# Kernel tuning notes

Measured on AMD Instinct MI355X. Metric: run time of the kernel, lower is better.

## Reference

```python
import jax, jax.numpy as jnp
import numpy as np

DIM = 384
HEADS = 8


def conv1x1(x, w):
    # x: [b,c,h,w], w: [o,c] (1x1 conv, no bias)
    return jnp.einsum('bchw,oc->bohw', x, w)


def dwconv3x3(x, w):
    # depthwise 3x3, padding=1. x: [b,c,h,w], w: [c,1,3,3]
    return jax.lax.conv_general_dilated(
        x, w, window_strides=(1, 1), padding='SAME',
        feature_group_count=x.shape[1],
        dimension_numbers=('NCHW', 'OIHW', 'NCHW'))


def l2norm(x, eps=1e-12):
    # F.normalize(dim=-1): x / max(||x||_2, eps)
    n = jnp.sqrt(jnp.sum(x * x, axis=-1, keepdims=True))
    return x / jnp.maximum(n, eps)


def topm_softmax(attn, m):
    # keep top-m per row (by value threshold == scatter of topk indices), -inf elsewhere
    thr = jax.lax.top_k(attn, m)[0][..., -1:]
    return jax.nn.softmax(jnp.where(attn >= thr, attn, -jnp.inf), axis=-1)


def setup_inputs() -> dict:
    key = jax.random.key(0)
    ks = jax.random.split(key, 9)
    d = DIM
    return {
        'x_q': jax.random.normal(ks[0], (8, d, 128, 128), jnp.float32),
        'x_kv': jax.random.normal(ks[1], (8, d, 128, 128), jnp.float32),
        'q_w': jax.random.normal(ks[2], (d, d), jnp.float32) * 0.02,
        'q_dw': jax.random.normal(ks[3], (d, 1, 3, 3), jnp.float32) * 0.02,
        'kv_w': jax.random.normal(ks[4], (2 * d, d), jnp.float32) * 0.02,
        'kv_dw': jax.random.normal(ks[5], (2 * d, 1, 3, 3), jnp.float32) * 0.02,
        'proj_w': jax.random.normal(ks[6], (d, d), jnp.float32) * 0.02,
        'temperature': jnp.ones((HEADS, 1, 1), jnp.float32),
        'a_mix': jnp.full((4,), 0.2, jnp.float32),  # attn1..attn4
    }


def reference(x_q, x_kv, q_w, q_dw, kv_w, kv_dw, proj_w, temperature, a_mix):
    b, c, h, w = x_q.shape
    C = c // HEADS  # channels per head
    n = h * w

    q = dwconv3x3(conv1x1(x_q, q_w), q_dw)
    kv = dwconv3x3(conv1x1(x_kv, kv_w), kv_dw)
    k, v = jnp.split(kv, 2, axis=1)

    q = l2norm(q.reshape(b, HEADS, C, n))
    k = l2norm(k.reshape(b, HEADS, C, n))
    v = v.reshape(b, HEADS, C, n)

    attn = jnp.einsum('bhcn,bhdn->bhcd', q, k) * temperature  # [b,H,C,C]

    topks = (C // 2, (2 * C) // 3, (3 * C) // 4, (4 * C) // 5)
    out = jnp.zeros_like(v)
    for i, m in enumerate(topks):
        a = topm_softmax(attn, m)
        out = out + a_mix[i] * jnp.einsum('bhcd,bhdn->bhcn', a, v)

    out = out.reshape(b, c, h, w)
    return conv1x1(out, proj_w)
```

## Files before the change

kernel.cpp:

```cpp
#include <hip/hip_runtime.h>
#include <cstdint>
#include <cstddef>

#define DIM 384
#define HEADS 8
#define NBATCH 8
#define NPIX 16384
#define CPH 48

typedef unsigned short h16_t;
typedef __attribute__((ext_vector_type(8))) _Float16 half8;
typedef __attribute__((ext_vector_type(4))) float floatx4;

__device__ __forceinline__ h16_t f2h(float f) {
  _Float16 h = (_Float16)f;
  return __builtin_bit_cast(h16_t, h);
}
__device__ __forceinline__ float h2f(h16_t u) {
  return (float)__builtin_bit_cast(_Float16, u);
}

__device__ __forceinline__ void gload_lds16(const void* g, void* l) {
  __builtin_amdgcn_global_load_lds(
      (const __attribute__((address_space(1))) unsigned int*)g,
      (__attribute__((address_space(3))) unsigned int*)l, 16, 0, 0);
}

__global__ void convert_h16_kernel(const float* __restrict__ in, h16_t* __restrict__ out, int n) {
  int i = blockIdx.x * blockDim.x + threadIdx.x;
  if (i < n) out[i] = f2h(in[i]);
}

template <typename T>
__global__ __launch_bounds__(256) void transpose_conv_kernel(
    const T* __restrict__ in, h16_t* __restrict__ out, int C, int Nn) {
  __shared__ h16_t tile[64][68];
  int b = blockIdx.z;
  int c0 = blockIdx.y * 64;
  int n0 = blockIdx.x * 64;
  const T* src = in + (size_t)b * C * Nn;
  h16_t* dst = out + (size_t)b * Nn * C;
  int t = threadIdx.x;
  int cl = t >> 4;
  int n4 = (t & 15) << 2;
#pragma unroll
  for (int p = 0; p < 4; ++p) {
    int c = cl + p * 16;
    const T* sp = src + (size_t)(c0 + c) * Nn + n0 + n4;
    h16_t v0, v1, v2, v3;
    if (sizeof(T) == 4) {
      float4 f = *(const float4*)sp;
      v0 = f2h(f.x); v1 = f2h(f.y); v2 = f2h(f.z); v3 = f2h(f.w);
    } else {
      ushort4 u = *(const ushort4*)sp;
      v0 = u.x; v1 = u.y; v2 = u.z; v3 = u.w;
    }
    tile[n4 + 0][c] = v0;
    tile[n4 + 1][c] = v1;
    tile[n4 + 2][c] = v2;
    tile[n4 + 3][c] = v3;
  }
  __syncthreads();
  int nl = t >> 4;
  int c4 = (t & 15) << 2;
#pragma unroll
  for (int p = 0; p < 4; ++p) {
    int n = nl + p * 16;
    ushort4 w;
    w.x = tile[n][c4 + 0];
    w.y = tile[n][c4 + 1];
    w.z = tile[n][c4 + 2];
    w.w = tile[n][c4 + 3];
    *(ushort4*)(dst + (size_t)(n0 + n) * C + c0 + c4) = w;
  }
}

template <bool F32OUT, bool ABATCH>
__global__ __launch_bounds__(256) void gemm_bt_kernel(
    const h16_t* __restrict__ Aall, const h16_t* __restrict__ Ball, void* __restrict__ Cout) {
  __shared__ __align__(16) h16_t lds[16384];
  h16_t* lA = lds;
  h16_t* lB = lds + 8192;
  int b = blockIdx.z, mb = blockIdx.y, nb = blockIdx.x;
  const h16_t* A = Aall + (ABATCH ? (size_t)b * DIM * DIM : (size_t)0) + (size_t)mb * 128 * DIM;
  const h16_t* B = Ball + ((size_t)b * NPIX + (size_t)nb * 128) * DIM;
  int tid = threadIdx.x;
  int wid = tid >> 6, lane = tid & 63;
  int wi = wid >> 1, wj = wid & 1;
  int quad = lane >> 4, l15 = lane & 15;
  int srow = lane >> 3;
  int schunk = (lane & 7) ^ srow;

  floatx4 acc[4][4];
#pragma unroll
  for (int i = 0; i < 4; ++i)
#pragma unroll
    for (int j = 0; j < 4; ++j) acc[i][j] = (floatx4)0.0f;

  for (int kt = 0; kt < 6; ++kt) {
    __syncthreads();
#pragma unroll
    for (int t = 0; t < 4; ++t) {
      int r = (wid * 4 + t) * 8 + srow;
      const h16_t* ga = A + (size_t)r * DIM + kt * 64 + schunk * 8;
      const h16_t* gb = B + (size_t)r * DIM + kt * 64 + schunk * 8;
      char* la = (char*)lA + (wid * 4 + t) * 1024 + lane * 16;
      char* lb = (char*)lB + (wid * 4 + t) * 1024 + lane * 16;
      gload_lds16(ga, la);
      gload_lds16(gb, lb);
    }
    __syncthreads();
#pragma unroll
    for (int ks = 0; ks < 2; ++ks) {
      half8 af[4], bfr[4];
      int ph = (((ks << 2) | quad) ^ (l15 & 7)) << 4;
#pragma unroll
      for (int i = 0; i < 4; ++i)
        af[i] = *(const half8*)((const char*)lA + (wi * 64 + i * 16 + l15) * 128 + ph);
#pragma unroll
      for (int j = 0; j < 4; ++j)
        bfr[j] = *(const half8*)((const char*)lB + (wj * 64 + j * 16 + l15) * 128 + ph);
#pragma unroll
      for (int i = 0; i < 4; ++i)
#pragma unroll
        for (int j = 0; j < 4; ++j)
          acc[i][j] = __builtin_amdgcn_mfma_f32_16x16x32_f16(af[i], bfr[j], acc[i][j], 0, 0, 0);
    }
  }
  int orow0 = mb * 128 + wi * 64 + quad * 4;
  int ncol0 = nb * 128 + wj * 64 + l15;
#pragma unroll
  for (int i = 0; i < 4; ++i) {
#pragma unroll
    for (int j = 0; j < 4; ++j) {
#pragma unroll
      for (int r = 0; r < 4; ++r) {
        size_t idx = ((size_t)b * DIM + (orow0 + i * 16 + r)) * NPIX + (ncol0 + j * 16);
        if (F32OUT)
          ((float*)Cout)[idx] = acc[i][j][r];
        else
          ((h16_t*)Cout)[idx] = f2h(acc[i][j][r]);
      }
    }
  }
}

__device__ __forceinline__ void load_row6(const h16_t* ip, int yy, int x0, float* r) {
  if ((unsigned)yy > 127u) {
    r[0] = r[1] = r[2] = r[3] = r[4] = r[5] = 0.f;
    return;
  }
  const h16_t* row = ip + (yy << 7) + x0;
  ushort4 m = *(const ushort4*)row;
  r[0] = (x0 > 0) ? h2f(row[-1]) : 0.f;
  r[1] = h2f(m.x); r[2] = h2f(m.y); r[3] = h2f(m.z); r[4] = h2f(m.w);
  r[5] = (x0 < 124) ? h2f(row[4]) : 0.f;
}

__global__ __launch_bounds__(256) void dwconv_kernel(
    const h16_t* __restrict__ in, const float* __restrict__ wbase,
    h16_t* __restrict__ out, float* __restrict__ norm2) {
  int c = blockIdx.x, b = blockIdx.y;
  const h16_t* ip = in + ((size_t)(b * DIM + c) << 14);
  h16_t* op = out + ((size_t)(b * DIM + c) << 14);
  const float* wp = wbase + c * 9;
  float w0 = wp[0], w1 = wp[1], w2 = wp[2], w3 = wp[3], w4 = wp[4];
  float w5 = wp[5], w6 = wp[6], w7 = wp[7], w8 = wp[8];
  float ssum = 0.f;
  for (int t = threadIdx.x; t < 4096; t += 256) {
    int y = t >> 5;
    int x0 = (t & 31) << 2;
    float r0[6], r1[6], r2[6];
    load_row6(ip, y - 1, x0, r0);
    load_row6(ip, y,     x0, r1);
    load_row6(ip, y + 1, x0, r2);
    ushort4 st;
#pragma unroll
    for (int i = 0; i < 4; ++i) {
      float o = w0 * r0[i] + w1 * r0[i + 1] + w2 * r0[i + 2]
              + w3 * r1[i] + w4 * r1[i + 1] + w5 * r1[i + 2]
              + w6 * r2[i] + w7 * r2[i + 1] + w8 * r2[i + 2];
      h16_t ob = f2h(o);
      float of = h2f(ob);
      ssum += of * of;
      if (i == 0) st.x = ob; else if (i == 1) st.y = ob; else if (i == 2) st.z = ob; else st.w = ob;
    }
    *(ushort4*)(op + (y << 7) + x0) = st;
  }
  if (norm2 != nullptr) {
    __shared__ float red[256];
    int tid = threadIdx.x;
    red[tid] = ssum;
    __syncthreads();
    for (int s = 128; s > 0; s >>= 1) {
      if (tid < s) red[tid] += red[tid + s];
      __syncthreads();
    }
    if (tid == 0) norm2[b * DIM + c] = red[0];
  }
}

__global__ __launch_bounds__(64) void attn_gemm_kernel(
    const h16_t* __restrict__ q, const h16_t* __restrict__ k, float* __restrict__ attn) {
  int chunk = blockIdx.x, bh = blockIdx.y;
  int b = bh >> 3, h = bh & 7;
  const h16_t* qb = q + ((size_t)(b * DIM + h * CPH) << 14);
  const h16_t* kb = k + ((size_t)(b * DIM + h * CPH) << 14);
  int lane = threadIdx.x;
  int quad = lane >> 4, l15 = lane & 15;
  int off0 = chunk * 2048 + quad * 8;
  floatx4 acc[3][3];
#pragma unroll
  for (int i = 0; i < 3; ++i)
#pragma unroll
    for (int j = 0; j < 3; ++j) acc[i][j] = (floatx4)0.0f;
  for (int s = 0; s < 64; ++s) {
    int off = off0 + s * 32;
    half8 af[3], bfr[3];
#pragma unroll
    for (int i = 0; i < 3; ++i) {
      af[i]  = *(const half8*)(qb + ((size_t)(i * 16 + l15) << 14) + off);
      bfr[i] = *(const half8*)(kb + ((size_t)(i * 16 + l15) << 14) + off);
    }
#pragma unroll
    for (int i = 0; i < 3; ++i)
#pragma unroll
      for (int j = 0; j < 3; ++j)
        acc[i][j] = __builtin_amdgcn_mfma_f32_16x16x32_f16(af[i], bfr[j], acc[i][j], 0, 0, 0);
  }
  float* ap = attn + (size_t)bh * CPH * CPH;
#pragma unroll
  for (int i = 0; i < 3; ++i)
#pragma unroll
    for (int j = 0; j < 3; ++j)
#pragma unroll
      for (int r = 0; r < 4; ++r)
        atomicAdd(&ap[(i * 16 + quad * 4 + r) * CPH + j * 16 + l15], acc[i][j][r]);
}

__global__ __launch_bounds__(256) void combine_kernel(
    const float* __restrict__ attn, const float* __restrict__ n2q, const float* __restrict__ n2k,
    const float* __restrict__ temp, const float* __restrict__ amix,
    const float* __restrict__ projw, h16_t* __restrict__ Bmat) {
  int bh = blockIdx.x;
  int b = bh >> 3, h = bh & 7;
  __shared__ float Asc[CPH][CPH];
  __shared__ float Ex[CPH][CPH];
  __shared__ float thr[CPH][4];
  __shared__ float rmax[CPH];
  __shared__ float den[CPH][4];
  __shared__ float rsq[CPH], rsk[CPH];
  int tid = threadIdx.x;
  if (tid < CPH) {
    float nq = sqrtf(n2q[b * DIM + h * CPH + tid]);
    rsq[tid] = 1.f / fmaxf(nq, 1e-12f);
    float nk = sqrtf(n2k[b * DIM + h * CPH + tid]);
    rsk[tid] = 1.f / fmaxf(nk, 1e-12f);
  }
  __syncthreads();
  float tscale = temp[h];
  const float* ap = attn + (size_t)bh * CPH * CPH;
  for (int idx = tid; idx < CPH * CPH; idx += 256) {
    int c = idx / CPH, d = idx - c * CPH;
    Asc[c][d] = ap[idx] * rsq[c] * rsk[d] * tscale;
  }
  __syncthreads();
  const int M0 = 24, M1 = 32, M2 = 36, M3 = 38;
  for (int idx = tid; idx < CPH * CPH; idx += 256) {
    int c = idx / CPH, d = idx - c * CPH;
    float a = Asc[c][d];
    int gt = 0, ge = 0;
    float mx = -1e30f;
    for (int e = 0; e < CPH; ++e) {
      float v = Asc[c][e];
      gt += (v > a);
      ge += (v >= a);
      mx = fmaxf(mx, v);
    }
    if (d == 0) rmax[c] = mx;
    if (gt < M0 && ge >= M0) thr[c][0] = a;
    if (gt < M1 && ge >= M1) thr[c][1] = a;
    if (gt < M2 && ge >= M2) thr[c][2] = a;
    if (gt < M3 && ge >= M3) thr[c][3] = a;
  }
  __syncthreads();
  for (int idx = tid; idx < CPH * CPH; idx += 256) {
    int c = idx / CPH, d = idx - c * CPH;
    Ex[c][d] = expf(Asc[c][d] - rmax[c]);
  }
  __syncthreads();
  if (tid < CPH * 4) {
    int c = tid >> 2, mi = tid & 3;
    float t_ = thr[c][mi];
    float s = 0.f;
    for (int e = 0; e < CPH; ++e)
      if (Asc[c][e] >= t_) s += Ex[c][e];
    den[c][mi] = s;
  }
  __syncthreads();
  float a0 = amix[0], a1 = amix[1], a2 = amix[2], a3 = amix[3];
  for (int idx = tid; idx < CPH * CPH; idx += 256) {
    int c = idx / CPH, d = idx - c * CPH;
    float a = Asc[c][d];
    float s = 0.f;
    if (a >= thr[c][0]) s += a0 / den[c][0];
    if (a >= thr[c][1]) s += a1 / den[c][1];
    if (a >= thr[c][2]) s += a2 / den[c][2];
    if (a >= thr[c][3]) s += a3 / den[c][3];
    Ex[c][d] = Ex[c][d] * s;
  }
  __syncthreads();
  for (int idx = tid; idx < DIM * CPH; idx += 256) {
    int o = idx / CPH, d = idx - (idx / CPH) * CPH;
    const float* pw = projw + (size_t)o * DIM + h * CPH;
    float s = 0.f;
    for (int c2 = 0; c2 < CPH; ++c2) s += pw[c2] * Ex[c2][d];
    Bmat[((size_t)b * DIM + o) * DIM + h * CPH + d] = f2h(s);
  }
}

extern "C" void kernel_launch(void* const* d_in, const int* in_sizes, int n_in,
                              void* d_out, int out_size, void* d_ws, size_t ws_size,
                              hipStream_t stream) {
  const float* x_q    = (const float*)d_in[0];
  const float* x_kv   = (const float*)d_in[1];
  const float* q_w    = (const float*)d_in[2];
  const float* q_dw   = (const float*)d_in[3];
  const float* kv_w   = (const float*)d_in[4];
  const float* kv_dw  = (const float*)d_in[5];
  const float* proj_w = (const float*)d_in[6];
  const float* temp   = (const float*)d_in[7];
  const float* amix   = (const float*)d_in[8];

  char* ws = (char*)d_ws;
  const size_t SLOT = (size_t)NBATCH * NPIX * DIM * 2;
  h16_t* S0 = (h16_t*)(ws);
  h16_t* S1 = (h16_t*)(ws + SLOT);
  h16_t* S2 = (h16_t*)(ws + 2 * SLOT);
  h16_t* S3 = (h16_t*)(ws + 3 * SLOT);
  char* p = ws + 4 * SLOT;
  h16_t* WqB  = (h16_t*)p; p += (size_t)DIM * DIM * 2;
  h16_t* WkvB = (h16_t*)p; p += (size_t)2 * DIM * DIM * 2;
  float* n2q  = (float*)p;  p += (size_t)NBATCH * DIM * 4;
  float* n2k  = (float*)p;  p += (size_t)NBATCH * DIM * 4;
  float* attn = (float*)p;  p += (size_t)64 * CPH * CPH * 4;
  h16_t* Bmat = (h16_t*)p; p += (size_t)NBATCH * DIM * DIM * 2;

  hipMemsetAsync(attn, 0, (size_t)64 * CPH * CPH * 4, stream);

  convert_h16_kernel<<<dim3((DIM * DIM + 255) / 256), 256, 0, stream>>>(q_w, WqB, DIM * DIM);
  convert_h16_kernel<<<dim3((2 * DIM * DIM + 255) / 256), 256, 0, stream>>>(kv_w, WkvB, 2 * DIM * DIM);

  dim3 tgrid(NPIX / 64, DIM / 64, NBATCH);
  dim3 ggrid(NPIX / 128, DIM / 128, NBATCH);

  transpose_conv_kernel<float><<<tgrid, 256, 0, stream>>>(x_q, S0, DIM, NPIX);
  gemm_bt_kernel<false, false><<<ggrid, 256, 0, stream>>>(WqB, S0, S1);
  dwconv_kernel<<<dim3(DIM, NBATCH), 256, 0, stream>>>(S1, q_dw, S2, n2q);

  transpose_conv_kernel<float><<<tgrid, 256, 0, stream>>>(x_kv, S0, DIM, NPIX);
  gemm_bt_kernel<false, false><<<ggrid, 256, 0, stream>>>(WkvB, S0, S1);
  dwconv_kernel<<<dim3(DIM, NBATCH), 256, 0, stream>>>(S1, kv_dw, S3, n2k);

  attn_gemm_kernel<<<dim3(8, 64), 64, 0, stream>>>(S2, S3, attn);
  combine_kernel<<<dim3(64), 256, 0, stream>>>(attn, n2q, n2k, temp, amix, proj_w, Bmat);

  gemm_bt_kernel<false, false><<<ggrid, 256, 0, stream>>>(WkvB + (size_t)DIM * DIM, S0, S1);
  dwconv_kernel<<<dim3(DIM, NBATCH), 256, 0, stream>>>(S1, kv_dw + (size_t)DIM * 9, S2, nullptr);
  transpose_conv_kernel<unsigned short><<<tgrid, 256, 0, stream>>>(S2, S3, DIM, NPIX);

  gemm_bt_kernel<true, true><<<ggrid, 256, 0, stream>>>(Bmat, S3, d_out);
}
```

Measured before the change: 1.190 ms.

## Fuse transposes into GEMM B-operand loads and double attention-GEMM grid

```diff
diff --git a/kernel.cpp b/kernel.cpp
--- a/kernel.cpp
+++ b/kernel.cpp
@@ -31,65 +31,35 @@
   if (i < n) out[i] = f2h(in[i]);
 }
 
-template <typename T>
-__global__ __launch_bounds__(256) void transpose_conv_kernel(
-    const T* __restrict__ in, h16_t* __restrict__ out, int C, int Nn) {
-  __shared__ h16_t tile[64][68];
-  int b = blockIdx.z;
-  int c0 = blockIdx.y * 64;
-  int n0 = blockIdx.x * 64;
-  const T* src = in + (size_t)b * C * Nn;
-  h16_t* dst = out + (size_t)b * Nn * C;
-  int t = threadIdx.x;
-  int cl = t >> 4;
-  int n4 = (t & 15) << 2;
-#pragma unroll
-  for (int p = 0; p < 4; ++p) {
-    int c = cl + p * 16;
-    const T* sp = src + (size_t)(c0 + c) * Nn + n0 + n4;
-    h16_t v0, v1, v2, v3;
-    if (sizeof(T) == 4) {
-      float4 f = *(const float4*)sp;
-      v0 = f2h(f.x); v1 = f2h(f.y); v2 = f2h(f.z); v3 = f2h(f.w);
-    } else {
-      ushort4 u = *(const ushort4*)sp;
-      v0 = u.x; v1 = u.y; v2 = u.z; v3 = u.w;
-    }
-    tile[n4 + 0][c] = v0;
-    tile[n4 + 1][c] = v1;
-    tile[n4 + 2][c] = v2;
-    tile[n4 + 3][c] = v3;
-  }
-  __syncthreads();
-  int nl = t >> 4;
-  int c4 = (t & 15) << 2;
-#pragma unroll
-  for (int p = 0; p < 4; ++p) {
-    int n = nl + p * 16;
-    ushort4 w;
-    w.x = tile[n][c4 + 0];
-    w.y = tile[n][c4 + 1];
-    w.z = tile[n][c4 + 2];
-    w.w = tile[n][c4 + 3];
-    *(ushort4*)(dst + (size_t)(n0 + n) * C + c0 + c4) = w;
-  }
-}
-
-template <bool F32OUT, bool ABATCH>
-__global__ __launch_bounds__(256) void gemm_bt_kernel(
-    const h16_t* __restrict__ Aall, const h16_t* __restrict__ Ball, void* __restrict__ Cout) {
-  __shared__ __align__(16) h16_t lds[16384];
-  h16_t* lA = lds;
-  h16_t* lB = lds + 8192;
+template <bool F32OUT, bool ABATCH, typename BT>
+__global__ __launch_bounds__(256) void gemm_tn_kernel(
+    const h16_t* __restrict__ Aall, const BT* __restrict__ Ball, void* __restrict__ Cout) {
+  __shared__ __align__(16) h16_t lA[128 * 64];
+  __shared__ __align__(16) h16_t lB[128 * 72];
   int b = blockIdx.z, mb = blockIdx.y, nb = blockIdx.x;
   const h16_t* A = Aall + (ABATCH ? (size_t)b * DIM * DIM : (size_t)0) + (size_t)mb * 128 * DIM;
-  const h16_t* B = Ball + ((size_t)b * NPIX + (size_t)nb * 128) * DIM;
+  const BT* B = Ball + (size_t)b * DIM * NPIX + (size_t)nb * 128;
   int tid = threadIdx.x;
   int wid = tid >> 6, lane = tid & 63;
   int wi = wid >> 1, wj = wid & 1;
   int quad = lane >> 4, l15 = lane & 15;
   int srow = lane >> 3;
   int schunk = (lane & 7) ^ srow;
+  int koct = tid & 7;
+  int n4 = tid >> 3;
+
+  float4 f[8];
+  ushort4 u[8];
+  auto loadB = [&](int ktL) {
+    const BT* bp = B + (size_t)(ktL * 64 + koct * 8) * NPIX + (size_t)n4 * 4;
+#pragma unroll
+    for (int i = 0; i < 8; ++i) {
+      if constexpr (sizeof(BT) == 4)
+        f[i] = *(const float4*)(bp + (size_t)i * NPIX);
+      else
+        u[i] = *(const ushort4*)(bp + (size_t)i * NPIX);
+    }
+  };
 
   floatx4 acc[4][4];
 #pragma unroll
@@ -97,29 +67,48 @@
 #pragma unroll
     for (int j = 0; j < 4; ++j) acc[i][j] = (floatx4)0.0f;
 
+  loadB(0);
   for (int kt = 0; kt < 6; ++kt) {
     __syncthreads();
+    half8 w0, w1, w2, w3;
+#pragma unroll
+    for (int i = 0; i < 8; ++i) {
+      if constexpr (sizeof(BT) == 4) {
+        w0[i] = (_Float16)f[i].x; w1[i] = (_Float16)f[i].y;
+        w2[i] = (_Float16)f[i].z; w3[i] = (_Float16)f[i].w;
+      } else {
+        w0[i] = __builtin_bit_cast(_Float16, u[i].x);
+        w1[i] = __builtin_bit_cast(_Float16, u[i].y);
+        w2[i] = __builtin_bit_cast(_Float16, u[i].z);
+        w3[i] = __builtin_bit_cast(_Float16, u[i].w);
+      }
+    }
+    {
+      char* bb = (char*)lB + n4 * (4 * 144) + koct * 16;
+      *(half8*)(bb + 0)   = w0;
+      *(half8*)(bb + 144) = w1;
+      *(half8*)(bb + 288) = w2;
+      *(half8*)(bb + 432) = w3;
+    }
 #pragma unroll
     for (int t = 0; t < 4; ++t) {
       int r = (wid * 4 + t) * 8 + srow;
-      const h16_t* ga = A + (size_t)r * DIM + kt * 64 + schunk * 8;
-      const h16_t* gb = B + (size_t)r * DIM + kt * 64 + schunk * 8;
-      char* la = (char*)lA + (wid * 4 + t) * 1024 + lane * 16;
-      char* lb = (char*)lB + (wid * 4 + t) * 1024 + lane * 16;
-      gload_lds16(ga, la);
-      gload_lds16(gb, lb);
+      gload_lds16(A + (size_t)r * DIM + kt * 64 + schunk * 8,
+                  (char*)lA + (wid * 4 + t) * 1024 + lane * 16);
     }
     __syncthreads();
+    if (kt < 5) loadB(kt + 1);
 #pragma unroll
     for (int ks = 0; ks < 2; ++ks) {
       half8 af[4], bfr[4];
       int ph = (((ks << 2) | quad) ^ (l15 & 7)) << 4;
+      int pb = (((ks << 2) | quad)) << 4;
 #pragma unroll
       for (int i = 0; i < 4; ++i)
         af[i] = *(const half8*)((const char*)lA + (wi * 64 + i * 16 + l15) * 128 + ph);
 #pragma unroll
       for (int j = 0; j < 4; ++j)
-        bfr[j] = *(const half8*)((const char*)lB + (wj * 64 + j * 16 + l15) * 128 + ph);
+        bfr[j] = *(const half8*)((const char*)lB + (wj * 64 + j * 16 + l15) * 144 + pb);
 #pragma unroll
       for (int i = 0; i < 4; ++i)
 #pragma unroll
@@ -208,13 +197,13 @@
   const h16_t* kb = k + ((size_t)(b * DIM + h * CPH) << 14);
   int lane = threadIdx.x;
   int quad = lane >> 4, l15 = lane & 15;
-  int off0 = chunk * 2048 + quad * 8;
+  int off0 = chunk * 1024 + quad * 8;
   floatx4 acc[3][3];
 #pragma unroll
   for (int i = 0; i < 3; ++i)
 #pragma unroll
     for (int j = 0; j < 3; ++j) acc[i][j] = (floatx4)0.0f;
-  for (int s = 0; s < 64; ++s) {
+  for (int s = 0; s < 32; ++s) {
     int off = off0 + s * 32;
     half8 af[3], bfr[3];
 #pragma unroll
@@ -351,23 +340,19 @@
   convert_h16_kernel<<<dim3((DIM * DIM + 255) / 256), 256, 0, stream>>>(q_w, WqB, DIM * DIM);
   convert_h16_kernel<<<dim3((2 * DIM * DIM + 255) / 256), 256, 0, stream>>>(kv_w, WkvB, 2 * DIM * DIM);
 
-  dim3 tgrid(NPIX / 64, DIM / 64, NBATCH);
   dim3 ggrid(NPIX / 128, DIM / 128, NBATCH);
 
-  transpose_conv_kernel<float><<<tgrid, 256, 0, stream>>>(x_q, S0, DIM, NPIX);
-  gemm_bt_kernel<false, false><<<ggrid, 256, 0, stream>>>(WqB, S0, S1);
-  dwconv_kernel<<<dim3(DIM, NBATCH), 256, 0, stream>>>(S1, q_dw, S2, n2q);
-
-  transpose_conv_kernel<float><<<tgrid, 256, 0, stream>>>(x_kv, S0, DIM, NPIX);
-  gemm_bt_kernel<false, false><<<ggrid, 256, 0, stream>>>(WkvB, S0, S1);
-  dwconv_kernel<<<dim3(DIM, NBATCH), 256, 0, stream>>>(S1, kv_dw, S3, n2k);
-
-  attn_gemm_kernel<<<dim3(8, 64), 64, 0, stream>>>(S2, S3, attn);
+  gemm_tn_kernel<false, false, float><<<ggrid, 256, 0, stream>>>(WqB, x_q, S0);
+  dwconv_kernel<<<dim3(DIM, NBATCH), 256, 0, stream>>>(S0, q_dw, S2, n2q);
+
+  gemm_tn_kernel<false, false, float><<<ggrid, 256, 0, stream>>>(WkvB, x_kv, S0);
+  gemm_tn_kernel<false, false, float><<<ggrid, 256, 0, stream>>>(WkvB + (size_t)DIM * DIM, x_kv, S1);
+  dwconv_kernel<<<dim3(DIM, NBATCH), 256, 0, stream>>>(S0, kv_dw, S3, n2k);
+
+  attn_gemm_kernel<<<dim3(16, 64), 64, 0, stream>>>(S2, S3, attn);
   combine_kernel<<<dim3(64), 256, 0, stream>>>(attn, n2q, n2k, temp, amix, proj_w, Bmat);
 
-  gemm_bt_kernel<false, false><<<ggrid, 256, 0, stream>>>(WkvB + (size_t)DIM * DIM, S0, S1);
   dwconv_kernel<<<dim3(DIM, NBATCH), 256, 0, stream>>>(S1, kv_dw + (size_t)DIM * 9, S2, nullptr);
-  transpose_conv_kernel<unsigned short><<<tgrid, 256, 0, stream>>>(S2, S3, DIM, NPIX);
-
-  gemm_bt_kernel<true, true><<<ggrid, 256, 0, stream>>>(Bmat, S3, d_out);
-}
+
+  gemm_tn_kernel<true, true, h16_t><<<ggrid, 256, 0, stream>>>(Bmat, S2, d_out);
+}
```

After: 1.231 ms. 3.5% more time.
